# Performance work log

Hardware: AMD Instinct MI355X
Metric: run time of the kernel (lower is better)

## Reference

```python
import jax, jax.numpy as jnp
import numpy as np

SUN = 9.0          # sudoku digit range constant (SuN in the repo)
N_HEAD = 8
D_MODEL = 128
CHUNK = 24         # query-chunk size for memory-efficient L1 distance (744 = 31*24)


def _qgelu(z):
    return z * jax.nn.sigmoid(1.702 * z)


def _l1_scores(q, k, scale):
    """a[b,s,d,h] = -sum_w |q[b,s,h,w] - k[b,d,h,w]| * scale, computed in query chunks
    to avoid the full [b,n,n,h,w] broadcast intermediate (mirrors the L1Attn CUDA kernel)."""
    b, n, h, w = q.shape
    nc = n // CHUNK
    qc = q.reshape(b, nc, CHUNK, h, w).transpose(1, 0, 2, 3, 4)  # [nc,b,c,h,w]

    def f(qi):
        # qi: [b,c,h,w] -> scores [b,c,n,h]
        return -jnp.abs(qi[:, :, None, :, :] - k[:, None, :, :, :]).sum(-1) * scale

    a = jax.lax.map(f, qc)                                        # [nc,b,c,n,h]
    return a.transpose(1, 0, 2, 3, 4).reshape(b, n, n, h)


def _forward(x, wk, wqv_w, wqv_b, fanin_w, fanin_b):
    b, n, w = x.shape
    h = N_HEAD
    # wqv: Linear(d_model -> 3*n_head*d_model), split into q, vf, vb
    v = (x @ wqv_w.T + wqv_b).reshape(b, n, 3 * h, w)
    q, vf, vb = v[:, :, :h, :], v[:, :, h:2 * h, :], v[:, :, 2 * h:, :]
    # k = x broadcast to heads, scaled by learned per-head wk
    k = x[:, :, None, :] * wk[None, None, :, :]                   # [b,n,h,w]

    # dense branch: L1 attention with an extra zero "null" logit, softmax over source dim
    a = _l1_scores(q, k, 1.0 / np.sqrt(w))                        # [b,s,d,h]
    a = jnp.concatenate([a, jnp.zeros((b, 1, n, h), a.dtype)], axis=1)  # zero row at s=n
    a = jax.nn.softmax(a, axis=1)[:, :n]                          # [b,s,d,h]

    # bidirectional value combine: forward (vf) and backward (vb)
    bf = jnp.einsum('bsdh,bshw->bdhw', a, vf)
    bb = jnp.einsum('bdsh,bshw->bdhw', a, vb)
    y = (bf + bb).sum(axis=2)                                     # sum over heads -> [b,n,w]

    y = _qgelu(y + SUN / 2.0) - SUN / 2.0
    y = y @ fanin_w.T + fanin_b
    return x + y


def setup_inputs() -> dict:
    key = jax.random.key(0)
    k0, k1, k2 = jax.random.split(key, 3)
    b, n = 4, 744  # ntok NOT a multiple of 16 (code asserts padn > 0)
    x = jax.random.normal(k0, (b, n, D_MODEL), jnp.float32)
    wk = 0.005 * jnp.ones((N_HEAD, D_MODEL), jnp.float32)
    wqv_w = 0.005 * jax.random.normal(k1, (3 * N_HEAD * D_MODEL, D_MODEL), jnp.float32)
    wqv_b = jnp.zeros((3 * N_HEAD * D_MODEL,), jnp.float32)
    fanin_w = 0.005 * jax.random.normal(k2, (D_MODEL, D_MODEL), jnp.float32)
    fanin_b = jnp.zeros((D_MODEL,), jnp.float32)
    return {"x": x, "wk": wk, "wqv_w": wqv_w, "wqv_b": wqv_b,
            "fanin_w": fanin_w, "fanin_b": fanin_b, "layer": 0, "pas": 0}


def reference(x, wk, wqv_w, wqv_b, fanin_w, fanin_b, layer, pas):
    # hcoo = ['dense'] is hardcoded; layer/pas select the (single) dense branch.
    return _forward(x, wk, wqv_w, wqv_b, fanin_w, fanin_b)
```

## Files before the change

kernel.cpp:

```cpp
#include <hip/hip_runtime.h>
#include <hip/hip_bf16.h>
#include <cstdint>

#define N_TOK 744
#define NP    768
#define DW    128
#define NH    8

typedef __attribute__((ext_vector_type(4))) float f32x4;
typedef __attribute__((ext_vector_type(4))) unsigned int u32x4;
typedef __attribute__((ext_vector_type(8))) __bf16 bf16x8;
typedef __attribute__((ext_vector_type(4))) __bf16 bf16x4;

__device__ __forceinline__ unsigned int sadu8(unsigned int a, unsigned int b, unsigned int c) {
    unsigned int d;
    asm("v_sad_u8 %0, %1, %2, %3" : "=v"(d) : "v"(a), "v"(b), "v"(c));
    return d;
}

__global__ void k_zinit(float* Z, int n) {
    int i = blockIdx.x * 256 + threadIdx.x;
    if (i < n) Z[i] = 1.0f;
}

__global__ __launch_bounds__(256) void k_proj(
    const float* __restrict__ x, const float* __restrict__ wqv_w,
    const float* __restrict__ wqv_b,
    float* __restrict__ qbuf, __bf16* __restrict__ vf_t, __bf16* __restrict__ vb_t,
    int M)
{
    int tid = threadIdx.x;
    int l = tid & 63, wv = tid >> 6;
    int lr = l & 15, lg = l >> 4;
    int mbase = blockIdx.y * 64 + wv * 16;
    int c0 = blockIdx.x * 64;
    bool vpath = (c0 >= 1024);
    f32x4 acc[4] = {};
    for (int kk = 0; kk < 128; kk += 32) {
        int ka = kk + lg * 8;
        int ra = mbase + lr; if (ra >= M) ra = 0;
        const float* ap = x + (size_t)ra * DW + ka;
        float a0[8];
        *(f32x4*)a0 = *(const f32x4*)ap; *(f32x4*)(a0 + 4) = *(const f32x4*)(ap + 4);
        bf16x8 af;
        for (int j = 0; j < 8; j++) af[j] = (__bf16)a0[j];
        for (int ct = 0; ct < 4; ct++) {
            int cb = c0 + ct * 16 + lr;
            const float* bp = wqv_w + (size_t)cb * DW + ka;
            float b0[8];
            *(f32x4*)b0 = *(const f32x4*)bp; *(f32x4*)(b0 + 4) = *(const f32x4*)(bp + 4);
            bf16x8 bfr;
            for (int j = 0; j < 8; j++) bfr[j] = (__bf16)b0[j];
            if (vpath) acc[ct] = __builtin_amdgcn_mfma_f32_16x16x32_bf16(bfr, af, acc[ct], 0, 0, 0);
            else       acc[ct] = __builtin_amdgcn_mfma_f32_16x16x32_bf16(af, bfr, acc[ct], 0, 0, 0);
        }
    }
    if (!vpath) {
        for (int ct = 0; ct < 4; ct++) {
            int c = c0 + ct * 16 + lr;
            int hd = c >> 7, wi = c & 127;
            float bias = wqv_b[c];
            for (int j = 0; j < 4; j++) {
                int r = mbase + lg * 4 + j;
                if (r >= M) continue;
                int b = r / N_TOK, s = r % N_TOK;
                qbuf[(((size_t)b * NH + hd) * NP + s) * DW + wi] = acc[ct][j] + bias;
            }
        }
    } else {
        int r = mbase + lr;
        bool rok = (r < M);
        int b = rok ? (r / N_TOK) : 0;
        int st = rok ? (r % N_TOK) : 0;
        int hd0 = c0 >> 7;
        __bf16* dst0 = (hd0 < 16) ? vf_t : vb_t;
        int hh = (hd0 < 16) ? (hd0 - 8) : (hd0 - 16);
        for (int ct = 0; ct < 4; ct++) {
            int cb = c0 + ct * 16 + lg * 4;
            f32x4 bias4 = *(const f32x4*)(wqv_b + cb);
            for (int j = 0; j < 4; j++) {
                int wi = (cb + j) & 127;
                if (rok)
                    dst0[(((size_t)b * NH + hh) * DW + wi) * NP + st] =
                        (__bf16)(acc[ct][j] + bias4[j]);
            }
        }
    }
}

__global__ __launch_bounds__(256) void k_scores(
    const float* __restrict__ qbuf, const float* __restrict__ x,
    const float* __restrict__ wk,
    __bf16* __restrict__ e1, __bf16* __restrict__ e2, float* __restrict__ Z)
{
    __shared__ unsigned int qt[32][132];
    __shared__ unsigned int kt[32][132];
    int bh = blockIdx.z; int b = bh >> 3, h = bh & 7;
    int s0 = blockIdx.y * 128, d0 = blockIdx.x * 128;
    int tid = threadIdx.x;
    int ty = tid >> 4, tx = tid & 15;
    const float* qbase = qbuf + (size_t)bh * NP * DW;
    const float* xbase = x + (size_t)b * N_TOK * DW;
    const float* wkh = wk + h * DW;

    int cg = tid & 31;
    int r0 = tid >> 5;
    float w4[4];
    *(f32x4*)w4 = *(const f32x4*)(wkh + 4 * cg);
    const float CL = 0.9921875f;
    #pragma unroll
    for (int pass = 0; pass < 16; pass++) {
        int r = pass * 8 + r0;
        f32x4 qv4 = *(const f32x4*)(qbase + (size_t)(s0 + r) * DW + 4 * cg);
        unsigned int uq = 0;
        #pragma unroll
        for (int e = 0; e < 4; e++) {
            float v = fminf(fmaxf(qv4[e], -CL), CL);
            unsigned int u = (unsigned int)__builtin_fmaf(v, 128.0f, 128.5f);
            uq |= u << (8 * e);
        }
        qt[cg][r] = uq;
        int d = d0 + r;
        f32x4 xv4 = {};
        if (d < N_TOK) xv4 = *(const f32x4*)(xbase + (size_t)d * DW + 4 * cg);
        unsigned int uk = 0;
        #pragma unroll
        for (int e = 0; e < 4; e++) {
            float v = fminf(fmaxf(xv4[e] * w4[e], -CL), CL);
            unsigned int u = (unsigned int)__builtin_fmaf(v, 128.0f, 128.5f);
            uk |= u << (8 * e);
        }
        kt[cg][r] = uk;
    }
    __syncthreads();

    unsigned int acc[8][8] = {};
    #pragma unroll 4
    for (int g = 0; g < 32; g++) {
        unsigned int qv[8], kv[8];
        *(u32x4*)&qv[0] = *(const u32x4*)&qt[g][ty * 8];
        *(u32x4*)&qv[4] = *(const u32x4*)&qt[g][ty * 8 + 4];
        *(u32x4*)&kv[0] = *(const u32x4*)&kt[g][tx * 8];
        *(u32x4*)&kv[4] = *(const u32x4*)&kt[g][tx * 8 + 4];
        #pragma unroll
        for (int i = 0; i < 8; i++)
            #pragma unroll
            for (int j = 0; j < 8; j++)
                acc[i][j] = sadu8(qv[i], kv[j], acc[i][j]);
    }

    const float SS = 0.08838834764831845f / 128.0f;
    float e[8][8]; float colsum[8] = {};
    int sb = s0 + ty * 8, db = d0 + tx * 8;
    #pragma unroll
    for (int i = 0; i < 8; i++)
        #pragma unroll
        for (int j = 0; j < 8; j++) {
            float ev = ((sb + i) < N_TOK && (db + j) < N_TOK)
                       ? __expf(-(float)acc[i][j] * SS) : 0.0f;
            e[i][j] = ev; colsum[j] += ev;
        }
    size_t ebase = (size_t)bh * NP * NP;
    #pragma unroll
    for (int i = 0; i < 8; i++) {
        bf16x8 v;
        #pragma unroll
        for (int j = 0; j < 8; j++) v[j] = (__bf16)e[i][j];
        *(bf16x8*)&e2[ebase + (size_t)(sb + i) * NP + db] = v;
    }
    #pragma unroll
    for (int j = 0; j < 8; j++) {
        bf16x8 v;
        #pragma unroll
        for (int i = 0; i < 8; i++) v[i] = (__bf16)e[i][j];
        *(bf16x8*)&e1[ebase + (size_t)(db + j) * NP + sb] = v;
    }
    __syncthreads();
    float* red = (float*)&qt[0][0];
    #pragma unroll
    for (int j = 0; j < 8; j++) red[ty * 128 + tx * 8 + j] = colsum[j];
    __syncthreads();
    if (tid < 128) {
        float z = 0;
        #pragma unroll
        for (int r = 0; r < 16; r++) z += red[r * 128 + tid];
        atomicAdd(&Z[(size_t)bh * NP + d0 + tid], z);
    }
}

__global__ void k_scalevb(__bf16* vb_t, const float* __restrict__ Z, long total8)
{
    long idx = (long)blockIdx.x * blockDim.x + threadIdx.x;
    if (idx >= total8) return;
    size_t base = (size_t)idx * 8;
    int s = (int)(base % NP);
    int bh = (int)((base / NP) / DW);
    bf16x8 v = *(bf16x8*)&vb_t[base];
    const float* Zp = Z + (size_t)bh * NP + s;
    bf16x8 o;
    #pragma unroll
    for (int i = 0; i < 8; i++) o[i] = (__bf16)((float)v[i] / Zp[i]);
    *(bf16x8*)&vb_t[base] = o;
}

__global__ __launch_bounds__(256) void k_apply(
    const __bf16* __restrict__ e1, const __bf16* __restrict__ e2,
    const __bf16* __restrict__ vf_t, const __bf16* __restrict__ vb_t,
    const float* __restrict__ Z, __bf16* __restrict__ y0f, __bf16* __restrict__ y0b)
{
    __shared__ __align__(16) char smem[2][40960];
    int bh = blockIdx.y;
    int tid = threadIdx.x;
    int l = tid & 63, wv = tid >> 6;
    int lr = l & 15, lg = l >> 4;
    int m0b = blockIdx.x * 32;
    int m0 = m0b + (wv & 1) * 16;
    bool doF = (wv < 2);

    const char* e1b = (const char*)e1 + 2 * ((size_t)bh * NP * NP + (size_t)m0b * NP);
    const char* e2b = (const char*)e2 + 2 * ((size_t)bh * NP * NP + (size_t)m0b * NP);
    const char* vfb = (const char*)vf_t + 2 * ((size_t)bh * DW * NP);
    const char* vbb = (const char*)vb_t + 2 * ((size_t)bh * DW * NP);
    unsigned int swz = (16u * (l & 7)) ^ (((unsigned)(l >> 3)) << 4);
    size_t rowoff = (size_t)(l >> 3) * (NP * 2);

    #define STAGE(bi, kk) do {                                                        \
        for (int u = wv; u < 40; u += 4) {                                            \
            char* lp = &smem[bi][u * 1024];                                           \
            const char* gp;                                                           \
            if (u < 4)       gp = e1b + (size_t)(8 * u) * (NP * 2);                   \
            else if (u < 8)  gp = e2b + (size_t)(8 * (u - 4)) * (NP * 2);             \
            else if (u < 24) gp = vfb + (size_t)(8 * (u - 8)) * (NP * 2);             \
            else             gp = vbb + (size_t)(8 * (u - 24)) * (NP * 2);            \
            gp += rowoff + (size_t)(kk) * 2 + swz;                                    \
            __builtin_amdgcn_global_load_lds(                                         \
                (const __attribute__((address_space(1))) void*)gp,                    \
                (__attribute__((address_space(3))) void*)lp, 16, 0, 0);               \
        }                                                                             \
    } while (0)

    const char* eL0 = &smem[0][doF ? 0 : 4096];
    const char* vL0 = &smem[0][doF ? 8192 : 24576];
    int mloc = (wv & 1) * 16 + lr;
    unsigned int rswz = ((unsigned)(lr & 7)) << 4;

    f32x4 acc[8] = {};
    STAGE(0, 0);
    STAGE(1, 64);
    for (int t = 0; t < 12; t++) {
        if (t < 11) asm volatile("s_waitcnt vmcnt(10)" ::: "memory");
        else        asm volatile("s_waitcnt vmcnt(0)" ::: "memory");
        __builtin_amdgcn_s_barrier();
        const char* eL = eL0 + (t & 1) * 40960;
        const char* vL = vL0 + (t & 1) * 40960;
        #pragma unroll
        for (int ph = 0; ph < 2; ph++) {
            unsigned int csw = (ph * 64 + lg * 16) ^ rswz;
            bf16x8 a = *(const bf16x8*)(eL + mloc * 128 + csw);
            #pragma unroll
            for (int ct = 0; ct < 8; ct++) {
                bf16x8 bfr = *(const bf16x8*)(vL + (ct * 16 + lr) * 128 + csw);
                acc[ct] = __builtin_amdgcn_mfma_f32_16x16x32_bf16(a, bfr, acc[ct], 0, 0, 0);
            }
        }
        __builtin_amdgcn_s_barrier();
        if (t + 2 < 12) STAGE(t & 1, (t + 2) * 64);
    }
    #undef STAGE

    float sc[4];
    #pragma unroll
    for (int j = 0; j < 4; j++)
        sc[j] = doF ? (1.0f / Z[(size_t)bh * NP + m0 + lg * 4 + j]) : 1.0f;
    __bf16* yb = (doF ? y0f : y0b) + ((size_t)bh * NP + m0) * DW;
    #pragma unroll
    for (int ct = 0; ct < 8; ct++)
        #pragma unroll
        for (int j = 0; j < 4; j++)
            yb[(size_t)(lg * 4 + j) * DW + ct * 16 + lr] = (__bf16)(sc[j] * acc[ct][j]);
}

__global__ __launch_bounds__(256) void k_fin1(
    const __bf16* __restrict__ y0f, const __bf16* __restrict__ y0b,
    __bf16* __restrict__ g, int M)
{
    int idx = blockIdx.x * 256 + threadIdx.x;
    int r = idx >> 4;
    int c = (idx & 15) * 8;
    if (r >= M) return;
    int b = r / N_TOK, s = r % N_TOK;
    float sum[8] = {};
    size_t base = ((size_t)b * NH * NP + s) * DW + c;
    #pragma unroll
    for (int h = 0; h < NH; h++) {
        bf16x8 vf_ = *(const bf16x8*)&y0f[base + (size_t)h * NP * DW];
        bf16x8 vb_ = *(const bf16x8*)&y0b[base + (size_t)h * NP * DW];
        #pragma unroll
        for (int i = 0; i < 8; i++) sum[i] += (float)vf_[i] + (float)vb_[i];
    }
    bf16x8 o;
    #pragma unroll
    for (int i = 0; i < 8; i++) {
        float z = sum[i] + 4.5f;
        float gv = z / (1.0f + __expf(-1.702f * z)) - 4.5f;
        o[i] = (__bf16)gv;
    }
    *(bf16x8*)&g[(size_t)r * DW + c] = o;
}

__global__ __launch_bounds__(256) void k_fin2(
    const __bf16* __restrict__ g, const float* __restrict__ x,
    const float* __restrict__ fanin_w, const float* __restrict__ fanin_b,
    float* __restrict__ out, int M)
{
    int tid = threadIdx.x;
    int l = tid & 63, wv = tid >> 6;
    int lr = l & 15, lg = l >> 4;
    int m0 = blockIdx.x * 64 + wv * 16;
    f32x4 acc[8] = {};
    int ar = m0 + lr; if (ar >= M) ar = M - 1;
    const __bf16* gp = g + (size_t)ar * DW;
    for (int kk = 0; kk < 128; kk += 32) {
        int ko = kk + lg * 8;
        bf16x8 a = *(const bf16x8*)(gp + ko);
        #pragma unroll
        for (int ct = 0; ct < 8; ct++) {
            const float* wp = fanin_w + (size_t)(ct * 16 + lr) * DW + ko;
            float w0[8];
            *(f32x4*)w0 = *(const f32x4*)wp; *(f32x4*)(w0 + 4) = *(const f32x4*)(wp + 4);
            bf16x8 bfr;
            #pragma unroll
            for (int j2 = 0; j2 < 8; j2++) bfr[j2] = (__bf16)w0[j2];
            acc[ct] = __builtin_amdgcn_mfma_f32_16x16x32_bf16(a, bfr, acc[ct], 0, 0, 0);
        }
    }
    #pragma unroll
    for (int ct = 0; ct < 8; ct++) {
        int c = ct * 16 + lr;
        float fb = fanin_b[c];
        #pragma unroll
        for (int j = 0; j < 4; j++) {
            int r = m0 + lg * 4 + j;
            if (r < M) out[(size_t)r * DW + c] = x[(size_t)r * DW + c] + acc[ct][j] + fb;
        }
    }
}

extern "C" void kernel_launch(void* const* d_in, const int* in_sizes, int n_in,
                              void* d_out, int out_size, void* d_ws, size_t ws_size,
                              hipStream_t stream)
{
    const float* x       = (const float*)d_in[0];
    const float* wk      = (const float*)d_in[1];
    const float* wqv_w   = (const float*)d_in[2];
    const float* wqv_b   = (const float*)d_in[3];
    const float* fanin_w = (const float*)d_in[4];
    const float* fanin_b = (const float*)d_in[5];
    int B = in_sizes[0] / (N_TOK * DW);
    int M = B * N_TOK;

    char* ws = (char*)d_ws;
    size_t off = 0;
    float*  qbuf = (float*)(ws + off);  off += (size_t)B * NH * NP * DW * 4;
    __bf16* vf_t = (__bf16*)(ws + off); off += (size_t)B * NH * DW * NP * 2;
    __bf16* vb_t = (__bf16*)(ws + off); off += (size_t)B * NH * DW * NP * 2;
    __bf16* e1   = (__bf16*)(ws + off); off += (size_t)B * NH * NP * NP * 2;
    __bf16* e2   = (__bf16*)(ws + off); off += (size_t)B * NH * NP * NP * 2;
    float*  Z    = (float*)(ws + off);  off += (size_t)B * NH * NP * 4;
    __bf16* y0b  = (__bf16*)(ws + off); off += (size_t)B * NH * NP * DW * 2;
    if (off > ws_size) return;
    __bf16* y0f = (__bf16*)qbuf;
    __bf16* g   = vf_t;

    int zn = B * NH * NP;
    k_zinit<<<(zn + 255) / 256, 256, 0, stream>>>(Z, zn);

    dim3 gp(3072 / 64, (M + 63) / 64);
    k_proj<<<gp, 256, 0, stream>>>(x, wqv_w, wqv_b, qbuf, vf_t, vb_t, M);

    dim3 gs(NP / 128, NP / 128, B * NH);
    k_scores<<<gs, 256, 0, stream>>>(qbuf, x, wk, e1, e2, Z);

    long total8 = (long)B * NH * DW * NP / 8;
    k_scalevb<<<(int)((total8 + 255) / 256), 256, 0, stream>>>(vb_t, Z, total8);

    dim3 ga(NP / 32, B * NH);
    k_apply<<<ga, 256, 0, stream>>>(e1, e2, vf_t, vb_t, Z, y0f, y0b);

    int f1blocks = (M * (DW / 8) + 255) / 256;
    k_fin1<<<f1blocks, 256, 0, stream>>>(y0f, y0b, g, M);

    k_fin2<<<(M + 63) / 64, 256, 0, stream>>>(g, x, fanin_w, fanin_b, (float*)d_out, M);
}
```

Baseline: 235.5 us.

## Pre-convert projection inputs to bf16 and tile projection GEMM through LDS

Adds a conversion kernel that casts x and wqv_w to bf16 once into workspace. The projection kernel is rewritten to stage 128x128 bf16 tiles of both operands into LDS with direct global-to-LDS loads and an XOR swizzle, then compute 128x128 output tiles per block with MFMA, reusing each fragment across more outputs. This removes the repeated fp32 loads and per-lane conversions of the old 64x64 direct-from-global design, at the cost of an extra kernel launch, extra workspace traffic and 64KB of LDS per block, which limits occupancy.

```diff
diff --git a/kernel.cpp b/kernel.cpp
--- a/kernel.cpp
+++ b/kernel.cpp
@@ -23,68 +23,117 @@
     if (i < n) Z[i] = 1.0f;
 }
 
+__global__ __launch_bounds__(256) void k_cvt(
+    const float* __restrict__ x, const float* __restrict__ wqv_w,
+    __bf16* __restrict__ xb, __bf16* __restrict__ wb, int M, int Mp)
+{
+    int t = blockIdx.x * 256 + threadIdx.x;
+    int xgroups = Mp * 32;
+    if (t < xgroups) {
+        int r = t >> 5, c4 = (t & 31) * 4;
+        f32x4 v = {};
+        if (r < M) v = *(const f32x4*)(x + (size_t)r * DW + c4);
+        bf16x4 o;
+        #pragma unroll
+        for (int i = 0; i < 4; i++) o[i] = (__bf16)v[i];
+        *(bf16x4*)&xb[(size_t)r * DW + c4] = o;
+    } else if (t < xgroups + 3072 * 32) {
+        int t2 = t - xgroups;
+        int r = t2 >> 5, c4 = (t2 & 31) * 4;
+        f32x4 v = *(const f32x4*)(wqv_w + (size_t)r * DW + c4);
+        bf16x4 o;
+        #pragma unroll
+        for (int i = 0; i < 4; i++) o[i] = (__bf16)v[i];
+        *(bf16x4*)&wb[(size_t)r * DW + c4] = o;
+    }
+}
+
 __global__ __launch_bounds__(256) void k_proj(
-    const float* __restrict__ x, const float* __restrict__ wqv_w,
+    const __bf16* __restrict__ xb, const __bf16* __restrict__ wb,
     const float* __restrict__ wqv_b,
     float* __restrict__ qbuf, __bf16* __restrict__ vf_t, __bf16* __restrict__ vb_t,
     int M)
 {
-    int tid = threadIdx.x;
-    int l = tid & 63, wv = tid >> 6;
+    __shared__ __align__(16) char smem[65536];
+    int bx = blockIdx.x, by = blockIdx.y;
+    int tid = threadIdx.x, l = tid & 63, wv = tid >> 6;
     int lr = l & 15, lg = l >> 4;
-    int mbase = blockIdx.y * 64 + wv * 16;
-    int c0 = blockIdx.x * 64;
-    bool vpath = (c0 >= 1024);
-    f32x4 acc[4] = {};
-    for (int kk = 0; kk < 128; kk += 32) {
-        int ka = kk + lg * 8;
-        int ra = mbase + lr; if (ra >= M) ra = 0;
-        const float* ap = x + (size_t)ra * DW + ka;
-        float a0[8];
-        *(f32x4*)a0 = *(const f32x4*)ap; *(f32x4*)(a0 + 4) = *(const f32x4*)(ap + 4);
-        bf16x8 af;
-        for (int j = 0; j < 8; j++) af[j] = (__bf16)a0[j];
-        for (int ct = 0; ct < 4; ct++) {
-            int cb = c0 + ct * 16 + lr;
-            const float* bp = wqv_w + (size_t)cb * DW + ka;
-            float b0[8];
-            *(f32x4*)b0 = *(const f32x4*)bp; *(f32x4*)(b0 + 4) = *(const f32x4*)(bp + 4);
-            bf16x8 bfr;
-            for (int j = 0; j < 8; j++) bfr[j] = (__bf16)b0[j];
-            if (vpath) acc[ct] = __builtin_amdgcn_mfma_f32_16x16x32_bf16(bfr, af, acc[ct], 0, 0, 0);
-            else       acc[ct] = __builtin_amdgcn_mfma_f32_16x16x32_bf16(af, bfr, acc[ct], 0, 0, 0);
-        }
-    }
+    bool vpath = (bx >= 8);
+
+    const char* xg = (const char*)xb + (size_t)by * 128 * 256;
+    const char* wg = (const char*)wb + (size_t)bx * 128 * 256;
+
+    #pragma unroll
+    for (int u = wv; u < 64; u += 4) {
+        int row = 4 * (u & 31) + (l >> 4);
+        unsigned int chunk = (unsigned int)(l & 15) ^ (unsigned int)(row & 7);
+        const char* gp = (u < 32 ? xg : wg) + (size_t)row * 256 + chunk * 16;
+        char* lp = &smem[u * 1024];
+        __builtin_amdgcn_global_load_lds(
+            (const __attribute__((address_space(1))) void*)gp,
+            (__attribute__((address_space(3))) void*)lp, 16, 0, 0);
+    }
+    asm volatile("s_waitcnt vmcnt(0)" ::: "memory");
+    __builtin_amdgcn_s_barrier();
+
+    const char* Xt = smem;
+    const char* Wt = smem + 32768;
+    const char* TA = vpath ? Wt : Xt;
+    const char* TB = vpath ? Xt : Wt;
+
+    f32x4 acc[2][8] = {};
+    #pragma unroll
+    for (int kk = 0; kk < 4; kk++) {
+        int cA = kk * 4 + lg;
+        bf16x8 a[2];
+        #pragma unroll
+        for (int mr = 0; mr < 2; mr++) {
+            int row = wv * 32 + mr * 16 + lr;
+            a[mr] = *(const bf16x8*)(TA + row * 256 + (cA ^ (row & 7)) * 16);
+        }
+        #pragma unroll
+        for (int nc = 0; nc < 8; nc++) {
+            int row = nc * 16 + lr;
+            bf16x8 bfr = *(const bf16x8*)(TB + row * 256 + (cA ^ (row & 7)) * 16);
+            acc[0][nc] = __builtin_amdgcn_mfma_f32_16x16x32_bf16(a[0], bfr, acc[0][nc], 0, 0, 0);
+            acc[1][nc] = __builtin_amdgcn_mfma_f32_16x16x32_bf16(a[1], bfr, acc[1][nc], 0, 0, 0);
+        }
+    }
+
     if (!vpath) {
-        for (int ct = 0; ct < 4; ct++) {
-            int c = c0 + ct * 16 + lr;
-            int hd = c >> 7, wi = c & 127;
-            float bias = wqv_b[c];
+        int hd = bx;
+        #pragma unroll
+        for (int nc = 0; nc < 8; nc++) {
+            int wi = nc * 16 + lr;
+            float bias = wqv_b[bx * 128 + wi];
+            #pragma unroll
+            for (int mr = 0; mr < 2; mr++)
+                #pragma unroll
+                for (int j = 0; j < 4; j++) {
+                    int r = by * 128 + wv * 32 + mr * 16 + lg * 4 + j;
+                    if (r >= M) continue;
+                    int b = r / N_TOK, s = r % N_TOK;
+                    qbuf[(((size_t)b * NH + hd) * NP + s) * DW + wi] = acc[mr][nc][j] + bias;
+                }
+        }
+    } else {
+        __bf16* dst0 = (bx < 16) ? vf_t : vb_t;
+        int hh = (bx < 16) ? (bx - 8) : (bx - 16);
+        #pragma unroll
+        for (int mr = 0; mr < 2; mr++)
+            #pragma unroll
             for (int j = 0; j < 4; j++) {
-                int r = mbase + lg * 4 + j;
-                if (r >= M) continue;
-                int b = r / N_TOK, s = r % N_TOK;
-                qbuf[(((size_t)b * NH + hd) * NP + s) * DW + wi] = acc[ct][j] + bias;
+                int wi = wv * 32 + mr * 16 + lg * 4 + j;
+                float bias = wqv_b[bx * 128 + wi];
+                #pragma unroll
+                for (int nc = 0; nc < 8; nc++) {
+                    int r = by * 128 + nc * 16 + lr;
+                    if (r >= M) continue;
+                    int b = r / N_TOK, st = r % N_TOK;
+                    dst0[(((size_t)b * NH + hh) * DW + wi) * NP + st] =
+                        (__bf16)(acc[mr][nc][j] + bias);
+                }
             }
-        }
-    } else {
-        int r = mbase + lr;
-        bool rok = (r < M);
-        int b = rok ? (r / N_TOK) : 0;
-        int st = rok ? (r % N_TOK) : 0;
-        int hd0 = c0 >> 7;
-        __bf16* dst0 = (hd0 < 16) ? vf_t : vb_t;
-        int hh = (hd0 < 16) ? (hd0 - 8) : (hd0 - 16);
-        for (int ct = 0; ct < 4; ct++) {
-            int cb = c0 + ct * 16 + lg * 4;
-            f32x4 bias4 = *(const f32x4*)(wqv_b + cb);
-            for (int j = 0; j < 4; j++) {
-                int wi = (cb + j) & 127;
-                if (rok)
-                    dst0[(((size_t)b * NH + hh) * DW + wi) * NP + st] =
-                        (__bf16)(acc[ct][j] + bias4[j]);
-            }
-        }
     }
 }
 
@@ -358,6 +407,7 @@
     const float* fanin_b = (const float*)d_in[5];
     int B = in_sizes[0] / (N_TOK * DW);
     int M = B * N_TOK;
+    int Mp = ((M + 127) / 128) * 128;
 
     char* ws = (char*)d_ws;
     size_t off = 0;
@@ -368,6 +418,8 @@
     __bf16* e2   = (__bf16*)(ws + off); off += (size_t)B * NH * NP * NP * 2;
     float*  Z    = (float*)(ws + off);  off += (size_t)B * NH * NP * 4;
     __bf16* y0b  = (__bf16*)(ws + off); off += (size_t)B * NH * NP * DW * 2;
+    __bf16* xb   = (__bf16*)(ws + off); off += (size_t)Mp * DW * 2;
+    __bf16* wb   = (__bf16*)(ws + off); off += (size_t)3072 * DW * 2;
     if (off > ws_size) return;
     __bf16* y0f = (__bf16*)qbuf;
     __bf16* g   = vf_t;
@@ -375,8 +427,11 @@
     int zn = B * NH * NP;
     k_zinit<<<(zn + 255) / 256, 256, 0, stream>>>(Z, zn);
 
-    dim3 gp(3072 / 64, (M + 63) / 64);
-    k_proj<<<gp, 256, 0, stream>>>(x, wqv_w, wqv_b, qbuf, vf_t, vb_t, M);
+    int cvt_threads = (Mp + 3072) * 32;
+    k_cvt<<<(cvt_threads + 255) / 256, 256, 0, stream>>>(x, wqv_w, xb, wb, M, Mp);
+
+    dim3 gp(24, Mp / 128);
+    k_proj<<<gp, 256, 0, stream>>>(xb, wb, wqv_b, qbuf, vf_t, vb_t, M);
 
     dim3 gs(NP / 128, NP / 128, B * NH);
     k_scores<<<gs, 256, 0, stream>>>(qbuf, x, wk, e1, e2, Z);
```

After: 211.3 us. 10.3% less time.
